# Performance work log

Hardware: AMD Instinct MI355X
Metric: run time of the kernel (lower is better)

The kernel has to match this reference:

```python
import jax, jax.numpy as jnp
import numpy as np

FP4_CODE = np.array([-6, -4, -3, -2, -1.5, -1, -0.5, -0.0,
                     0.0, 0.5, 1, 1.5, 2, 3, 4, 6], dtype=np.float32)


def setup_inputs() -> dict:
    key = jax.random.key(0)
    k1, k2 = jax.random.split(key)
    rows, cols = 4096, 4096
    x = jax.random.normal(k1, (rows, cols), dtype=jnp.float32)
    # per-row positive scale, as produced by find_params (abs-max / (maxq/2)); keep away from 0
    scale = jax.random.uniform(k2, (rows, 1), dtype=jnp.float32, minval=0.1, maxval=1.0)
    code = jnp.asarray(FP4_CODE)  # 16-entry fp4 codebook from configure(bits=4)
    return {"x": x, "scale": scale, "code": code}


def reference(x, scale, code):
    # q = x / scale; nearest codeword by absolute distance; dequantize by scale
    q = x / scale                                   # [R, C]
    dist = jnp.abs(q[..., None] - code)             # [R, C, 16] broadcasted distance
    idx = jnp.argmin(dist, axis=-1)                 # [R, C] (first min on ties, like torch)
    xq = code[idx] * scale                          # gather + rescale
    return xq
```

## Files before the change

kernel.cpp:

```cpp
#include <hip/hip_runtime.h>


typedef float f4 __attribute__((ext_vector_type(4)));

__global__ __launch_bounds__(256) void fp4_quant_kernel(
    const float* __restrict__ x,
    const float* __restrict__ scale,
    float* __restrict__ out,
    int n16,
    int row_shift,
    int col_mask,
    int cols4)
{
    const int tid = blockIdx.x * blockDim.x + threadIdx.x;
    if (tid >= n16) return;

    const int row = tid >> row_shift;
    const int col = tid & col_mask;
    const int tpr = col_mask + 1;

    const float s = scale[row];
    const float r = 1.0f / s;
    const float halfs = 0.5f * s;

    const f4* __restrict__ x4 =
        reinterpret_cast<const f4*>(x) + (long)row * cols4 + col;
    f4* __restrict__ o4 =
        reinterpret_cast<f4*>(out) + (long)row * cols4 + col;

    f4 xv[4];
#pragma unroll
    for (int k = 0; k < 4; ++k) xv[k] = x4[(long)k * tpr];

#pragma unroll
    for (int k = 0; k < 4; ++k) {
        f4 ov;
#pragma unroll
        for (int e = 0; e < 4; ++e) {
            const float a  = xv[k][e];
            const float q0 = a * r;
            const float q  = fmaf(r, fmaf(-s, q0, a), q0);

            float hk = __builtin_ceilf(fmaf(2.0f, q, -0.5f));
            hk = fminf(fmaxf(hk, -4.0f), 4.0f);

            float ko = __builtin_ceilf(q - 0.5f);
            ko = fminf(fmaxf(ko, -4.0f), 4.0f);

            float kv = (fabsf(ko) > 2.5f) ? (ko + ko) : hk;
            kv = (q >   5.0f) ?  12.0f : kv;
            kv = (q <= -5.0f) ? -12.0f : kv;

            ov[e] = kv * halfs;
        }
        __builtin_nontemporal_store(ov, &o4[(long)k * tpr]);
    }
}

extern "C" void kernel_launch(void* const* d_in, const int* in_sizes, int n_in,
                              void* d_out, int out_size, void* d_ws, size_t ws_size,
                              hipStream_t stream) {
    const float* x     = (const float*)d_in[0];
    const float* scale = (const float*)d_in[1];
    float* out         = (float*)d_out;

    const int n    = in_sizes[0];
    const int rows = in_sizes[1];
    const int cols = n / rows;
    const int cols4 = cols / 4;
    const int tpr  = cols / 16;

    int row_shift = 0;
    while ((1 << row_shift) < tpr) ++row_shift;
    const int col_mask = tpr - 1;

    const int n16 = n / 16;
    const int block = 256;
    const int grid = (n16 + block - 1) / block;
    fp4_quant_kernel<<<grid, block, 0, stream>>>(x, scale, out,
                                                 n16, row_shift, col_mask, cols4);
}
```

Before: 110.8 us.

## Precompute row reciprocals in a separate kernel and use one float4 per thread

Adds a small pre-kernel that writes 1/scale per row into workspace, so the main kernel loads the reciprocal instead of dividing. The main kernel now handles one float4 per thread rather than four strided float4s, which gives four times as many threads and simpler indexing. The trade-off is an extra kernel launch, a second per-row load, and less memory-level parallelism per thread.

Result: no change. 110.6 us (median of 2 runs) (-0.2%).

```diff
diff --git a/kernel.cpp b/kernel.cpp
--- a/kernel.cpp
+++ b/kernel.cpp
@@ -3,58 +3,50 @@
 
 typedef float f4 __attribute__((ext_vector_type(4)));
 
+__global__ __launch_bounds__(256) void recip_kernel(
+    const float* __restrict__ scale, float* __restrict__ rws, int rows)
+{
+    const int i = blockIdx.x * blockDim.x + threadIdx.x;
+    if (i < rows) rws[i] = 1.0f / scale[i];
+}
+
 __global__ __launch_bounds__(256) void fp4_quant_kernel(
     const float* __restrict__ x,
     const float* __restrict__ scale,
+    const float* __restrict__ rws,
     float* __restrict__ out,
-    int n16,
-    int row_shift,
-    int col_mask,
-    int cols4)
+    int n4,
+    int row_shift)
 {
-    const int tid = blockIdx.x * blockDim.x + threadIdx.x;
-    if (tid >= n16) return;
+    const int gid = blockIdx.x * blockDim.x + threadIdx.x;
+    if (gid >= n4) return;
 
-    const int row = tid >> row_shift;
-    const int col = tid & col_mask;
-    const int tpr = col_mask + 1;
-
+    const int row = gid >> row_shift;
     const float s = scale[row];
-    const float r = 1.0f / s;
+    const float r = rws[row];
     const float halfs = 0.5f * s;
 
-    const f4* __restrict__ x4 =
-        reinterpret_cast<const f4*>(x) + (long)row * cols4 + col;
-    f4* __restrict__ o4 =
-        reinterpret_cast<f4*>(out) + (long)row * cols4 + col;
+    const f4 xv = reinterpret_cast<const f4*>(x)[gid];
+    f4 ov;
+#pragma unroll
+    for (int e = 0; e < 4; ++e) {
+        const float a  = xv[e];
+        const float q0 = a * r;
+        const float q  = fmaf(r, fmaf(-s, q0, a), q0);
 
-    f4 xv[4];
-#pragma unroll
-    for (int k = 0; k < 4; ++k) xv[k] = x4[(long)k * tpr];
+        float hk = __builtin_ceilf(fmaf(2.0f, q, -0.5f));
+        hk = fminf(fmaxf(hk, -4.0f), 4.0f);
 
-#pragma unroll
-    for (int k = 0; k < 4; ++k) {
-        f4 ov;
-#pragma unroll
-        for (int e = 0; e < 4; ++e) {
-            const float a  = xv[k][e];
-            const float q0 = a * r;
-            const float q  = fmaf(r, fmaf(-s, q0, a), q0);
+        float ko = __builtin_ceilf(q - 0.5f);
+        ko = fminf(fmaxf(ko, -4.0f), 4.0f);
 
-            float hk = __builtin_ceilf(fmaf(2.0f, q, -0.5f));
-            hk = fminf(fmaxf(hk, -4.0f), 4.0f);
+        float kv = (fabsf(ko) > 2.5f) ? (ko + ko) : hk;
+        kv = (q >   5.0f) ?  12.0f : kv;
+        kv = (q <= -5.0f) ? -12.0f : kv;
 
-            float ko = __builtin_ceilf(q - 0.5f);
-            ko = fminf(fmaxf(ko, -4.0f), 4.0f);
-
-            float kv = (fabsf(ko) > 2.5f) ? (ko + ko) : hk;
-            kv = (q >   5.0f) ?  12.0f : kv;
-            kv = (q <= -5.0f) ? -12.0f : kv;
-
-            ov[e] = kv * halfs;
-        }
-        __builtin_nontemporal_store(ov, &o4[(long)k * tpr]);
+        ov[e] = kv * halfs;
     }
+    __builtin_nontemporal_store(ov, &reinterpret_cast<f4*>(out)[gid]);
 }
 
 extern "C" void kernel_launch(void* const* d_in, const int* in_sizes, int n_in,
@@ -63,20 +55,20 @@
     const float* x     = (const float*)d_in[0];
     const float* scale = (const float*)d_in[1];
     float* out         = (float*)d_out;
+    float* rws         = (float*)d_ws;
 
     const int n    = in_sizes[0];
     const int rows = in_sizes[1];
     const int cols = n / rows;
     const int cols4 = cols / 4;
-    const int tpr  = cols / 16;
 
     int row_shift = 0;
-    while ((1 << row_shift) < tpr) ++row_shift;
-    const int col_mask = tpr - 1;
+    while ((1 << row_shift) < cols4) ++row_shift;
 
-    const int n16 = n / 16;
+    recip_kernel<<<(rows + 255) / 256, 256, 0, stream>>>(scale, rws, rows);
+
+    const int n4 = n / 4;
     const int block = 256;
-    const int grid = (n16 + block - 1) / block;
-    fp4_quant_kernel<<<grid, block, 0, stream>>>(x, scale, out,
-                                                 n16, row_shift, col_mask, cols4);
+    const int grid = (n4 + block - 1) / block;
+    fp4_quant_kernel<<<grid, block, 0, stream>>>(x, scale, rws, out, n4, row_shift);
 }
```
